# Performance work log

Hardware: AMD Instinct MI355X
Metric: run time of the kernel (lower is better)

Reference implementation:

```python
import jax, jax.numpy as jnp
import numpy as np

EMBED_DIM = 256
NUM_HEADS = 4
LN_EPS = 1e-5


def setup_inputs() -> dict:
    b, n, e = 2, 4096, EMBED_DIM
    key = jax.random.key(0)
    ks = jax.random.split(key, 12)
    x = jax.random.normal(ks[0], (b, n, e), dtype=jnp.float32)
    # rotary cache: cos/sin of random angles, shape [2, b, n, e, 1]
    ang = jax.random.uniform(ks[1], (b, n, e, 1), dtype=jnp.float32) * (2 * np.pi)
    encoding = jnp.stack([jnp.cos(ang), jnp.sin(ang)], axis=0)
    s_e = 1.0 / np.sqrt(e)
    s_2e = 1.0 / np.sqrt(2 * e)
    Wqkv_w = jax.random.normal(ks[2], (3 * e, e), dtype=jnp.float32) * s_e
    Wqkv_b = jax.random.normal(ks[3], (3 * e,), dtype=jnp.float32) * s_e
    out_w = jax.random.normal(ks[4], (e, e), dtype=jnp.float32) * s_e
    out_b = jax.random.normal(ks[5], (e,), dtype=jnp.float32) * s_e
    ffn1_w = jax.random.normal(ks[6], (2 * e, 2 * e), dtype=jnp.float32) * s_2e
    ffn1_b = jax.random.normal(ks[7], (2 * e,), dtype=jnp.float32) * s_2e
    ln_g = jnp.ones((2 * e,), dtype=jnp.float32)
    ln_b = jnp.zeros((2 * e,), dtype=jnp.float32)
    ffn2_w = jax.random.normal(ks[8], (e, 2 * e), dtype=jnp.float32) * s_2e
    ffn2_b = jax.random.normal(ks[9], (e,), dtype=jnp.float32) * s_2e
    return {"x": x, "encoding": encoding, "Wqkv_w": Wqkv_w, "Wqkv_b": Wqkv_b,
            "out_w": out_w, "out_b": out_b, "ffn1_w": ffn1_w, "ffn1_b": ffn1_b,
            "ln_g": ln_g, "ln_b": ln_b, "ffn2_w": ffn2_w, "ffn2_b": ffn2_b}


def _forward(x, encoding, Wqkv_w, Wqkv_b, out_w, out_b, ffn1_w, ffn1_b, ln_g, ln_b, ffn2_w, ffn2_b):
    b, n, e = x.shape
    h = NUM_HEADS
    hd = e // h
    qkv = x @ Wqkv_w.T + Wqkv_b                      # [b,n,3e]
    qkv = qkv.reshape(b, n, e, 3)
    qk, v = qkv[..., :2], qkv[..., 2]                # [b,n,e,2], [b,n,e]
    # rotate_half: interpret e as (h, hd//2, 2) pairs, rotate within pairs
    r = qk.reshape(b, n, h, hd // 2, 2, 2)
    r = jnp.stack([-r[..., 1, :], r[..., 0, :]], axis=4).reshape(b, n, e, 2)
    qk = qk * encoding[0] + r * encoding[1]          # cached rotary emb
    q = qk[..., 0].reshape(b, n, h, hd)
    k = qk[..., 1].reshape(b, n, h, hd)
    vh = v.reshape(b, n, h, hd)
    scale = 1.0 / np.sqrt(hd).astype(np.float32)
    scores = jnp.einsum('bqhd,bkhd->bhqk', q, k) * scale
    attn = jax.nn.softmax(scores, axis=-1)
    ctx = jnp.einsum('bhqk,bkhd->bqhd', attn, vh).reshape(b, n, e)
    message = ctx @ out_w.T + out_b
    y = jnp.concatenate([x, message], axis=2)        # [b,n,2e]
    y = y @ ffn1_w.T + ffn1_b
    mu = jnp.mean(y, axis=-1, keepdims=True)
    var = jnp.mean(jnp.square(y - mu), axis=-1, keepdims=True)
    y = (y - mu) * jax.lax.rsqrt(var + LN_EPS) * ln_g + ln_b
    y = jax.nn.gelu(y, approximate=False)            # torch nn.GELU default = exact
    y = y @ ffn2_w.T + ffn2_b
    return x + y


def reference(x, encoding, Wqkv_w, Wqkv_b, out_w, out_b, ffn1_w, ffn1_b, ln_g, ln_b, ffn2_w, ffn2_b):
    return _forward(x, encoding, Wqkv_w, Wqkv_b, out_w, out_b, ffn1_w, ffn1_b, ln_g, ln_b, ffn2_w, ffn2_b)
```

## Files before the change

### kernel.cpp

```cpp
#include <hip/hip_runtime.h>
#include <hip/hip_bf16.h>

using u16 = unsigned short;
using u16x8 = __attribute__((ext_vector_type(8))) unsigned short;
using s16x4 = __attribute__((ext_vector_type(4))) short;
using s16x8 = __attribute__((ext_vector_type(8))) short;
using f32x4 = __attribute__((ext_vector_type(4))) float;

__device__ __forceinline__ f32x4 mfma16(s16x8 a, s16x8 b, f32x4 c) {
    return __builtin_amdgcn_mfma_f32_16x16x32_bf16(a, b, c, 0, 0, 0);
}

__device__ __forceinline__ u16 f2bf(float f) {
    union { float f; unsigned u; } v; v.f = f;
    unsigned r = v.u + 0x7FFFu + ((v.u >> 16) & 1u);
    return (u16)(r >> 16);
}

__device__ __forceinline__ unsigned cvt_pk_bf16(float lo, float hi) {
    unsigned r;
    asm("v_cvt_pk_bf16_f32 %0, %1, %2" : "=v"(r) : "v"(lo), "v"(hi));
    return r;
}

__device__ __forceinline__ float fast_exp2(float x) {
    float r;
    asm("v_exp_f32 %0, %1" : "=v"(r) : "v"(x));
    return r;
}

__device__ __forceinline__ unsigned pk2(u16 a, u16 b) {
    return (unsigned)a | ((unsigned)b << 16);
}

__device__ __forceinline__ float bf2f(u16 u) {
    union { unsigned u; float f; } v; v.u = ((unsigned)u) << 16;
    return v.f;
}

__device__ __forceinline__ void gload_lds16(const u16* g, u16* l) {
    __builtin_amdgcn_global_load_lds(
        (const __attribute__((address_space(1))) void*)g,
        (__attribute__((address_space(3))) void*)l, 16, 0, 0);
}

__global__ __launch_bounds__(256) void conv_kernel(
    const float* __restrict__ s0, const float* __restrict__ s1,
    const float* __restrict__ s2, const float* __restrict__ s3,
    const float* __restrict__ s4,
    u16* __restrict__ d0, u16* __restrict__ d1, u16* __restrict__ d2,
    u16* __restrict__ d3, u16* __restrict__ d4)
{
    int i = blockIdx.x * 256 + threadIdx.x;
    const float* s; u16* d; int off;
    if (i < 524288)      { s = s0; d = d0; off = i; }
    else if (i < 573440) { s = s1; d = d1; off = i - 524288; }
    else if (i < 589824) { s = s2; d = d2; off = i - 573440; }
    else if (i < 655360) { s = s3; d = d3; off = i - 589824; }
    else                 { s = s4; d = d4; off = i - 655360; }
    float4 f = ((const float4*)s)[off];
    ushort4 u;
    u.x = f2bf(f.x); u.y = f2bf(f.y); u.z = f2bf(f.z); u.w = f2bf(f.w);
    ((ushort4*)d)[off] = u;
}

__global__ __launch_bounds__(256) void prep_kernel(
    const float* __restrict__ wout, const float* __restrict__ w1,
    const float* __restrict__ outb, const float* __restrict__ b1,
    u16* __restrict__ woutT, float* __restrict__ b1p)
{
    int bid = blockIdx.x, tid = threadIdx.x;
    if (bid < 16) {
        __shared__ u16 ts[64][72];
        int tr = (bid >> 2) * 64, tc = (bid & 3) * 64;
        #pragma unroll
        for (int i = 0; i < 2; ++i) {
            int c = tid + 256 * i;
            int r = c >> 3, cg = c & 7;
            float4 fa = *(const float4*)(wout + (size_t)(tr + r) * 256 + tc + cg * 8);
            float4 fb = *(const float4*)(wout + (size_t)(tr + r) * 256 + tc + cg * 8 + 4);
            ts[r][cg * 8 + 0] = f2bf(fa.x); ts[r][cg * 8 + 1] = f2bf(fa.y);
            ts[r][cg * 8 + 2] = f2bf(fa.z); ts[r][cg * 8 + 3] = f2bf(fa.w);
            ts[r][cg * 8 + 4] = f2bf(fb.x); ts[r][cg * 8 + 5] = f2bf(fb.y);
            ts[r][cg * 8 + 6] = f2bf(fb.z); ts[r][cg * 8 + 7] = f2bf(fb.w);
        }
        __syncthreads();
        #pragma unroll
        for (int i = 0; i < 2; ++i) {
            int c = tid + 256 * i;
            int d = c >> 3, ng = c & 7;
            uint4 o4 = make_uint4(
                pk2(ts[ng*8+0][d], ts[ng*8+1][d]), pk2(ts[ng*8+2][d], ts[ng*8+3][d]),
                pk2(ts[ng*8+4][d], ts[ng*8+5][d]), pk2(ts[ng*8+6][d], ts[ng*8+7][d]));
            *(uint4*)(woutT + (size_t)(tc + d) * 256 + tr + ng * 8) = o4;
        }
    } else {
        #pragma unroll
        for (int h = 0; h < 2; ++h) {
            int n = tid + 256 * h;
            float acc = b1[n];
            const float* wr = w1 + (size_t)n * 512 + 256;
            for (int k = 0; k < 256; ++k) acc += wr[k] * outb[k];
            b1p[n] = acc;
        }
    }
}

template<int OUTMODE, bool SPLIT, bool SPLITW, bool RESID, bool BIAS, int BM>
__global__ __launch_bounds__(256) void gemm_kernel(
    const u16* __restrict__ A0, const u16* __restrict__ A1,
    const u16* __restrict__ W0, const u16* __restrict__ W1,
    const float* __restrict__ bias, const float* __restrict__ resid,
    float* __restrict__ outf, u16* __restrict__ outb,
    int M, int N, int K, int lda0, int lda1, int ldw0, int ldw1, int ldo)
{
    constexpr int MS = BM / 32;
    __shared__ u16 A_lds[3][BM][64];
    __shared__ u16 B_lds[3][64][64];
    const int tid = threadIdx.x;
    const int l = tid & 63, w = tid >> 6;
    const int lr = l & 15, lg = l >> 4;
    const int r7 = lr & 7;
    const int m0 = blockIdx.x * BM, n0 = blockIdx.y * 64;
    const int wm = (w >> 1) * (BM / 2), wn = (w & 1) * 32;

    const int lrow = l >> 3;
    const int swz = (l & 7) ^ lrow;
    const int arow = (BM / 4) * w + lrow;
    const int brow = 16 * w + lrow;

    #define STAGE_G(s, b)                                                     \
        do {                                                                  \
            int k0_ = 64 * (s);                                               \
            const u16* As_; int lda_; int ka_ = k0_;                          \
            if (SPLIT && k0_ >= 256) { As_ = A1; lda_ = lda1; ka_ = k0_ - 256; }\
            else { As_ = A0; lda_ = lda0; }                                   \
            const u16* Ws_; int ldw_; int kw_ = k0_;                          \
            if (SPLITW && k0_ >= 256) { Ws_ = W1; ldw_ = ldw1; kw_ = k0_ - 256; }\
            else { Ws_ = W0; ldw_ = ldw0; }                                   \
            _Pragma("unroll")                                                 \
            for (int i = 0; i < BM / 32; ++i)                                 \
                gload_lds16(As_ + (size_t)(m0 + arow + 8 * i) * lda_ + ka_ + swz * 8,\
                            &A_lds[b][(BM / 4) * w + 8 * i][0]);              \
            _Pragma("unroll")                                                 \
            for (int i = 0; i < 2; ++i)                                       \
                gload_lds16(Ws_ + (size_t)(n0 + brow + 8 * i) * ldw_ + kw_ + swz * 8,\
                            &B_lds[b][16 * w + 8 * i][0]);                    \
        } while (0)

    f32x4 acc[MS][2];
    #pragma unroll
    for (int i = 0; i < MS; ++i)
        #pragma unroll
        for (int j = 0; j < 2; ++j)
            acc[i][j] = (f32x4){0.f, 0.f, 0.f, 0.f};

    const int NS = K >> 6;
    int cur = 0, nxt = 1;
    STAGE_G(0, 0);

    for (int s = 0; s < NS; ++s) {
        if (s + 1 < NS) {
            STAGE_G(s + 1, nxt);
            if constexpr (BM == 128)
                asm volatile("s_waitcnt vmcnt(6)" ::: "memory");
            else
                asm volatile("s_waitcnt vmcnt(4)" ::: "memory");
        } else {
            asm volatile("s_waitcnt vmcnt(0)" ::: "memory");
        }
        __builtin_amdgcn_sched_barrier(0);
        __builtin_amdgcn_s_barrier();
        __builtin_amdgcn_sched_barrier(0);

        #pragma unroll
        for (int ks = 0; ks < 2; ++ks) {
            s16x8 af[MS], bfr[2];
            #pragma unroll
            for (int ms = 0; ms < MS; ++ms)
                af[ms] = *(const s16x8*)&A_lds[cur][wm + ms * 16 + lr]
                                              [((ks * 4 + lg) ^ r7) * 8];
            #pragma unroll
            for (int ns = 0; ns < 2; ++ns)
                bfr[ns] = *(const s16x8*)&B_lds[cur][wn + ns * 16 + lr]
                                               [((ks * 4 + lg) ^ r7) * 8];
            #pragma unroll
            for (int ms = 0; ms < MS; ++ms)
                #pragma unroll
                for (int ns = 0; ns < 2; ++ns)
                    acc[ms][ns] = mfma16(af[ms], bfr[ns], acc[ms][ns]);
        }
        cur = nxt;
        nxt = (nxt == 2) ? 0 : nxt + 1;
    }
    #undef STAGE_G

    #pragma unroll
    for (int ms = 0; ms < MS; ++ms) {
        #pragma unroll
        for (int ns = 0; ns < 2; ++ns) {
            int cg = n0 + wn + ns * 16 + lr;
            float bv = BIAS ? bias[cg] : 0.f;
            #pragma unroll
            for (int r = 0; r < 4; ++r) {
                int rg = m0 + wm + ms * 16 + lg * 4 + r;
                float val = acc[ms][ns][r] + bv;
                if (RESID) val += resid[(size_t)rg * N + cg];
                if (OUTMODE == 0) outf[(size_t)rg * ldo + cg] = val;
                else              outb[(size_t)rg * ldo + cg] = f2bf(val);
            }
        }
    }
}

__global__ __launch_bounds__(256) void rope_tv_kernel(
    const u16* __restrict__ qkv, const float* __restrict__ enc,
    u16* __restrict__ Qo, u16* __restrict__ Ko, u16* __restrict__ Vt)
{
    __shared__ u16 vt_lds[64][72];
    const int tid = threadIdx.x;
    const int bh = blockIdx.y, n0 = blockIdx.x * 64;
    const int b = bh >> 2, h = bh & 3;
    const float qs = 0.18033688011112042f;

    #pragma unroll
    for (int it = 0; it < 8; ++it) {
        int task = it * 256 + tid;
        int r = task >> 5, t = task & 31;
        size_t grow = (size_t)(b * 4096 + n0 + r);
        const u16* base = qkv + grow * 768 + 3 * (h * 64) + 6 * t;
        ushort2 a01 = *(const ushort2*)(base);
        ushort2 a23 = *(const ushort2*)(base + 2);
        ushort2 a45 = *(const ushort2*)(base + 4);
        float q0 = bf2f(a01.x), k0 = bf2f(a01.y);
        float q1 = bf2f(a23.y), k1 = bf2f(a45.x);
        const float* cb = enc + grow * 256 + h * 64 + 2 * t;
        float2 cosv = *(const float2*)cb;
        float2 sinv = *(const float2*)(cb + 2097152);
        float qr0 = (q0 * cosv.x - q1 * sinv.x) * qs;
        float qr1 = (q1 * cosv.y + q0 * sinv.y) * qs;
        float kr0 = k0 * cosv.x - k1 * sinv.x;
        float kr1 = k1 * cosv.y + k0 * sinv.y;
        size_t o = ((size_t)bh * 4096 + n0 + r) * 64 + 2 * t;
        *(unsigned*)(Qo + o) = cvt_pk_bf16(qr0, qr1);
        *(unsigned*)(Ko + o) = cvt_pk_bf16(kr0, kr1);
        vt_lds[r][2 * t]     = a23.x;
        vt_lds[r][2 * t + 1] = a45.y;
    }
    __syncthreads();
    #pragma unroll
    for (int i = 0; i < 2; ++i) {
        int c = tid + 256 * i;
        int d = c >> 3, ng = c & 7;
        int kb = ng >> 2, lg4 = ng & 3;
        int base = 32 * kb + 4 * lg4;
        unsigned w0 = pk2(vt_lds[base +  0][d], vt_lds[base +  1][d]);
        unsigned w1 = pk2(vt_lds[base +  2][d], vt_lds[base +  3][d]);
        unsigned w2 = pk2(vt_lds[base + 16][d], vt_lds[base + 17][d]);
        unsigned w3 = pk2(vt_lds[base + 18][d], vt_lds[base + 19][d]);
        uint4 o4 = make_uint4(w0, w1, w2, w3);
        *(uint4*)(Vt + ((size_t)bh * 64 + d) * 4096 + n0 + ng * 8) = o4;
    }
}

__global__ __launch_bounds__(256) void attn_kernel(
    const u16* __restrict__ Qp, const u16* __restrict__ Kp,
    const u16* __restrict__ Vtp, u16* __restrict__ Opart,
    float* __restrict__ Ssum)
{
    __shared__ u16 K_lds[2][64][64];
    __shared__ u16 V_lds[2][64][64];
    const int tid = threadIdx.x;
    const int l = tid & 63, w = tid >> 6;
    const int lr = l & 15, lg = l >> 4;
    const int r7 = lr & 7;
    const int bh = blockIdx.y, z = blockIdx.z;
    const int n0 = blockIdx.x * 128 + w * 32;

    const u16* Qb = Qp + ((size_t)bh * 4096 + n0) * 64;
    s16x8 qf[2][2];
    #pragma unroll
    for (int qt = 0; qt < 2; ++qt)
        #pragma unroll
        for (int dh = 0; dh < 2; ++dh)
            qf[qt][dh] = *(const s16x8*)(Qb + (qt * 16 + lr) * 64 + dh * 32 + lg * 8);

    const u16* Kb = Kp + (size_t)bh * 4096 * 64 + (size_t)z * 1024 * 64;
    const u16* Vb = Vtp + (size_t)bh * 64 * 4096 + z * 1024;

    const int xs0 = (lg ^ r7) * 8;
    const int xs1 = ((4 + lg) ^ r7) * 8;

    const int swz = (l & 7) ^ ((l >> 3) & 7);
    const int row0 = 16 * w + (l >> 3);
    const size_t koff0 = (size_t)row0 * 64 + swz * 8;
    const size_t koff1 = (size_t)(row0 + 8) * 64 + swz * 8;
    const size_t voff0 = (size_t)row0 * 4096 + swz * 8;
    const size_t voff1 = (size_t)(row0 + 8) * 4096 + swz * 8;

    #define STAGE(kt, b)                                                      \
        do {                                                                  \
            const u16* ks_ = Kb + (size_t)(kt) * 4096;                        \
            const u16* vs_ = Vb + (size_t)(kt) * 64;                          \
            gload_lds16(ks_ + koff0, &K_lds[b][16 * w][0]);                   \
            gload_lds16(ks_ + koff1, &K_lds[b][16 * w + 8][0]);               \
            gload_lds16(vs_ + voff0, &V_lds[b][16 * w][0]);                   \
            gload_lds16(vs_ + voff1, &V_lds[b][16 * w + 8][0]);               \
        } while (0)

    f32x4 O[2][4];
    #pragma unroll
    for (int qt = 0; qt < 2; ++qt)
        #pragma unroll
        for (int dv = 0; dv < 4; ++dv)
            O[qt][dv] = (f32x4){0.f, 0.f, 0.f, 0.f};
    f32x4 ssum[2];
    ssum[0] = (f32x4){0.f, 0.f, 0.f, 0.f};
    ssum[1] = (f32x4){0.f, 0.f, 0.f, 0.f};
    s16x8 ones;
    #pragma unroll
    for (int j = 0; j < 8; ++j) ones[j] = (short)0x3F80;

    STAGE(0, 0);
    __syncthreads();

    #define PHASE(kt, CB, DO_STAGE)                                           \
        do {                                                                  \
            if (DO_STAGE) STAGE((kt) + 1, (CB) ^ 1);                          \
            f32x4 S[2][4];                                                    \
            __builtin_amdgcn_s_setprio(1);                                    \
            _Pragma("unroll")                                                 \
            for (int v4 = 0; v4 < 4; ++v4) {                                  \
                const int krow = v4 * 16 + lr;                                \
                s16x8 kf0 = *(const s16x8*)&K_lds[CB][krow][xs0];             \
                s16x8 kf1 = *(const s16x8*)&K_lds[CB][krow][xs1];             \
                _Pragma("unroll")                                             \
                for (int qt = 0; qt < 2; ++qt) {                              \
                    f32x4 zz = (f32x4){-24.f, -24.f, -24.f, -24.f};           \
                    zz = mfma16(kf0, qf[qt][0], zz);                          \
                    zz = mfma16(kf1, qf[qt][1], zz);                          \
                    S[qt][v4] = zz;                                           \
                }                                                             \
            }                                                                 \
            __builtin_amdgcn_s_setprio(0);                                    \
            s16x8 pa[2][2];                                                   \
            _Pragma("unroll")                                                 \
            for (int qt = 0; qt < 2; ++qt) {                                  \
                float p[4][4];                                                \
                _Pragma("unroll")                                             \
                for (int v4 = 0; v4 < 4; ++v4)                                \
                    _Pragma("unroll")                                         \
                    for (int r = 0; r < 4; ++r)                               \
                        p[v4][r] = fast_exp2(S[qt][v4][r]);                   \
                _Pragma("unroll")                                             \
                for (int kb = 0; kb < 2; ++kb) {                              \
                    union { unsigned u[4]; s16x8 v; } pu;                     \
                    pu.u[0] = cvt_pk_bf16(p[2*kb][0],   p[2*kb][1]);          \
                    pu.u[1] = cvt_pk_bf16(p[2*kb][2],   p[2*kb][3]);          \
                    pu.u[2] = cvt_pk_bf16(p[2*kb+1][0], p[2*kb+1][1]);        \
                    pu.u[3] = cvt_pk_bf16(p[2*kb+1][2], p[2*kb+1][3]);        \
                    pa[qt][kb] = pu.v;                                        \
                }                                                             \
            }                                                                 \
            __builtin_amdgcn_s_setprio(1);                                    \
            _Pragma("unroll")                                                 \
            for (int dv = 0; dv < 4; ++dv) {                                  \
                const int vrow = 16 * dv + lr;                                \
                s16x8 vf0 = *(const s16x8*)&V_lds[CB][vrow][xs0];             \
                s16x8 vf1 = *(const s16x8*)&V_lds[CB][vrow][xs1];             \
                _Pragma("unroll")                                             \
                for (int qt = 0; qt < 2; ++qt) {                              \
                    O[qt][dv] = mfma16(pa[qt][0], vf0, O[qt][dv]);            \
                    O[qt][dv] = mfma16(pa[qt][1], vf1, O[qt][dv]);            \
                }                                                             \
            }                                                                 \
            _Pragma("unroll")                                                 \
            for (int qt = 0; qt < 2; ++qt) {                                  \
                ssum[qt] = mfma16(pa[qt][0], ones, ssum[qt]);                 \
                ssum[qt] = mfma16(pa[qt][1], ones, ssum[qt]);                 \
            }                                                                 \
            __builtin_amdgcn_s_setprio(0);                                    \
            __syncthreads();                                                  \
        } while (0)

    #pragma unroll 1
    for (int kt = 0; kt < 16; kt += 2) {
        PHASE(kt, 0, true);
        PHASE(kt + 1, 1, kt < 14);
    }
    #undef PHASE
    #undef STAGE

    u16* Ob = Opart + ((size_t)(z * 8 + bh) * 4096 + n0) * 64;
    #pragma unroll
    for (int qt = 0; qt < 2; ++qt)
        #pragma unroll
        for (int dv = 0; dv < 4; ++dv)
            #pragma unroll
            for (int r = 0; r < 4; ++r)
                Ob[(size_t)(qt * 16 + 4 * lg + r) * 64 + 16 * dv + lr] =
                    f2bf(O[qt][dv][r]);
    if (lr == 0) {
        #pragma unroll
        for (int qt = 0; qt < 2; ++qt) {
            float4 sv = make_float4(ssum[qt][0], ssum[qt][1],
                                    ssum[qt][2], ssum[qt][3]);
            *(float4*)&Ssum[(size_t)(z * 8 + bh) * 4096 + n0 + qt * 16 + 4 * lg] = sv;
        }
    }
}

__global__ __launch_bounds__(256) void combine_kernel(
    const u16* __restrict__ Opart, const float* __restrict__ Ssum,
    u16* __restrict__ ctx)
{
    int idx = blockIdx.x * 256 + threadIdx.x;
    int rr = idx >> 3;
    int dc = (idx & 7) * 8;
    float s = Ssum[rr] + Ssum[32768 + rr] + Ssum[65536 + rr] + Ssum[98304 + rr];
    float inv = 1.f / s;
    float acc[8];
    #pragma unroll
    for (int j = 0; j < 8; ++j) acc[j] = 0.f;
    #pragma unroll
    for (int z = 0; z < 4; ++z) {
        u16x8 ov = *(const u16x8*)(Opart + ((size_t)z * 32768 + rr) * 64 + dc);
        #pragma unroll
        for (int j = 0; j < 8; ++j) acc[j] += bf2f(ov[j]);
    }
    #pragma unroll
    for (int j = 0; j < 8; ++j) acc[j] *= inv;
    int bh = rr >> 12, n = rr & 4095;
    int b = bh >> 2, h = bh & 3;
    uint4 o4 = make_uint4(cvt_pk_bf16(acc[0], acc[1]), cvt_pk_bf16(acc[2], acc[3]),
                          cvt_pk_bf16(acc[4], acc[5]), cvt_pk_bf16(acc[6], acc[7]));
    *(uint4*)(ctx + ((size_t)(b * 4096 + n)) * 256 + h * 64 + dc) = o4;
}

__global__ __launch_bounds__(256) void ln_gelu_kernel(
    const u16* __restrict__ y, const float* __restrict__ g,
    const float* __restrict__ bta, u16* __restrict__ o)
{
    int row = blockIdx.x * 4 + (threadIdx.x >> 6);
    int l = threadIdx.x & 63;
    const u16* yr = y + (size_t)row * 512 + l * 8;
    u16x8 uv = *(const u16x8*)yr;
    float v[8];
    #pragma unroll
    for (int j = 0; j < 8; ++j) v[j] = bf2f(uv[j]);
    float s = 0.f;
    #pragma unroll
    for (int j = 0; j < 8; ++j) s += v[j];
    #pragma unroll
    for (int off = 32; off; off >>= 1) s += __shfl_xor(s, off, 64);
    float mu = s * (1.f / 512.f);
    float q = 0.f;
    #pragma unroll
    for (int j = 0; j < 8; ++j) { float t = v[j] - mu; q += t * t; }
    #pragma unroll
    for (int off = 32; off; off >>= 1) q += __shfl_xor(q, off, 64);
    float rs = rsqrtf(q * (1.f / 512.f) + 1e-5f);
    u16 u[8];
    #pragma unroll
    for (int j = 0; j < 8; ++j) {
        float t = (v[j] - mu) * rs * g[l * 8 + j] + bta[l * 8 + j];
        t = t * 0.5f * (1.f + erff(t * 0.70710678118654752f));
        u[j] = f2bf(t);
    }
    uint4 o4 = make_uint4(pk2(u[0], u[1]), pk2(u[2], u[3]),
                          pk2(u[4], u[5]), pk2(u[6], u[7]));
    *(uint4*)(o + (size_t)row * 512 + l * 8) = o4;
}

extern "C" void kernel_launch(void* const* d_in, const int* in_sizes, int n_in,
                              void* d_out, int out_size, void* d_ws, size_t ws_size,
                              hipStream_t stream) {
    (void)in_sizes; (void)n_in; (void)out_size; (void)ws_size;
    const float* x    = (const float*)d_in[0];
    const float* enc  = (const float*)d_in[1];
    const float* wqkv = (const float*)d_in[2];
    const float* bqkv = (const float*)d_in[3];
    const float* wout = (const float*)d_in[4];
    const float* bout = (const float*)d_in[5];
    const float* w1   = (const float*)d_in[6];
    const float* b1   = (const float*)d_in[7];
    const float* lng  = (const float*)d_in[8];
    const float* lnb  = (const float*)d_in[9];
    const float* w2   = (const float*)d_in[10];
    const float* b2   = (const float*)d_in[11];
    float* out = (float*)d_out;
    char* ws = (char*)d_ws;

    u16*   xb    = (u16*)(ws + 0);
    u16*   wqkvb = (u16*)(ws + 4194304);
    u16*   woutb = (u16*)(ws + 4587520);
    u16*   w1b   = (u16*)(ws + 4718592);
    u16*   w2b   = (u16*)(ws + 5242880);
    u16*   qkvb  = (u16*)(ws + 5505024);
    u16*   OpartB= (u16*)(ws + 5505024);
    u16*   y1bf  = (u16*)(ws + 5505024);
    float* Ssum  = (float*)(ws + 22282240);
    u16*   woutT = (u16*)(ws + 22806528);
    u16*   wprime= (u16*)(ws + 22937600);
    float* b1p   = (float*)(ws + 23199744);
    u16*   q     = (u16*)(ws + 30670848);
    u16*   k     = (u16*)(ws + 34865152);
    u16*   vt    = (u16*)(ws + 43253760);
    u16*   ybf   = q;
    u16*   ctx   = (u16*)(ws + 47448064);

    conv_kernel<<<2688, 256, 0, stream>>>(x, wqkv, wout, w1, w2,
                                          xb, wqkvb, woutb, w1b, w2b);
    prep_kernel<<<17, 256, 0, stream>>>(wout, w1, bout, b1, woutT, b1p);
    gemm_kernel<1, false, false, false, false, 64><<<dim3(8, 4), 256, 0, stream>>>(
        w1b + 256, nullptr, woutT, nullptr, nullptr, nullptr, nullptr, wprime,
        512, 256, 256, 512, 0, 256, 0, 256);
    gemm_kernel<1, false, false, false, true, 128><<<dim3(64, 12), 256, 0, stream>>>(
        xb, nullptr, wqkvb, nullptr, bqkv, nullptr, nullptr, qkvb,
        8192, 768, 256, 256, 0, 256, 0, 768);
    rope_tv_kernel<<<dim3(64, 8), 256, 0, stream>>>(qkvb, enc, q, k, vt);
    attn_kernel<<<dim3(32, 8, 4), 256, 0, stream>>>(q, k, vt, OpartB, Ssum);
    combine_kernel<<<1024, 256, 0, stream>>>(OpartB, Ssum, ctx);
    gemm_kernel<1, true, true, false, true, 128><<<dim3(64, 8), 256, 0, stream>>>(
        xb, ctx, w1b, wprime, b1p, nullptr, nullptr, y1bf,
        8192, 512, 512, 256, 256, 512, 256, 512);
    ln_gelu_kernel<<<2048, 256, 0, stream>>>(y1bf, lng, lnb, ybf);
    gemm_kernel<0, false, false, true, true, 64><<<dim3(128, 4), 256, 0, stream>>>(
        ybf, nullptr, w2b, nullptr, b2, x, out, nullptr,
        8192, 256, 512, 512, 0, 512, 0, 256);
}
```

Before: 132.9 us.

## Replace folded out-projection weights with an explicit out-projection GEMM

Removes the precomputed folding of the output projection into the first FFN weights (the prep kernel, the W1·Wout GEMM and the folded bias). It instead runs a separate out-projection GEMM from ctx to a bf16 message buffer, then feeds x and the message into the FFN1 GEMM with the original weights and bias. This drops two small weight-prep launches and the split-weight path in the GEMM. In exchange it adds an 8192x256x256 GEMM plus a round trip of the message tensor through memory.

```diff
diff --git a/kernel.cpp b/kernel.cpp
--- a/kernel.cpp
+++ b/kernel.cpp
@@ -64,55 +64,13 @@
     ((ushort4*)d)[off] = u;
 }
 
-__global__ __launch_bounds__(256) void prep_kernel(
-    const float* __restrict__ wout, const float* __restrict__ w1,
-    const float* __restrict__ outb, const float* __restrict__ b1,
-    u16* __restrict__ woutT, float* __restrict__ b1p)
-{
-    int bid = blockIdx.x, tid = threadIdx.x;
-    if (bid < 16) {
-        __shared__ u16 ts[64][72];
-        int tr = (bid >> 2) * 64, tc = (bid & 3) * 64;
-        #pragma unroll
-        for (int i = 0; i < 2; ++i) {
-            int c = tid + 256 * i;
-            int r = c >> 3, cg = c & 7;
-            float4 fa = *(const float4*)(wout + (size_t)(tr + r) * 256 + tc + cg * 8);
-            float4 fb = *(const float4*)(wout + (size_t)(tr + r) * 256 + tc + cg * 8 + 4);
-            ts[r][cg * 8 + 0] = f2bf(fa.x); ts[r][cg * 8 + 1] = f2bf(fa.y);
-            ts[r][cg * 8 + 2] = f2bf(fa.z); ts[r][cg * 8 + 3] = f2bf(fa.w);
-            ts[r][cg * 8 + 4] = f2bf(fb.x); ts[r][cg * 8 + 5] = f2bf(fb.y);
-            ts[r][cg * 8 + 6] = f2bf(fb.z); ts[r][cg * 8 + 7] = f2bf(fb.w);
-        }
-        __syncthreads();
-        #pragma unroll
-        for (int i = 0; i < 2; ++i) {
-            int c = tid + 256 * i;
-            int d = c >> 3, ng = c & 7;
-            uint4 o4 = make_uint4(
-                pk2(ts[ng*8+0][d], ts[ng*8+1][d]), pk2(ts[ng*8+2][d], ts[ng*8+3][d]),
-                pk2(ts[ng*8+4][d], ts[ng*8+5][d]), pk2(ts[ng*8+6][d], ts[ng*8+7][d]));
-            *(uint4*)(woutT + (size_t)(tc + d) * 256 + tr + ng * 8) = o4;
-        }
-    } else {
-        #pragma unroll
-        for (int h = 0; h < 2; ++h) {
-            int n = tid + 256 * h;
-            float acc = b1[n];
-            const float* wr = w1 + (size_t)n * 512 + 256;
-            for (int k = 0; k < 256; ++k) acc += wr[k] * outb[k];
-            b1p[n] = acc;
-        }
-    }
-}
-
-template<int OUTMODE, bool SPLIT, bool SPLITW, bool RESID, bool BIAS, int BM>
+template<int OUTMODE, bool SPLIT, bool RESID, bool BIAS, int BM>
 __global__ __launch_bounds__(256) void gemm_kernel(
     const u16* __restrict__ A0, const u16* __restrict__ A1,
-    const u16* __restrict__ W0, const u16* __restrict__ W1,
-    const float* __restrict__ bias, const float* __restrict__ resid,
-    float* __restrict__ outf, u16* __restrict__ outb,
-    int M, int N, int K, int lda0, int lda1, int ldw0, int ldw1, int ldo)
+    const u16* __restrict__ W0, const float* __restrict__ bias,
+    const float* __restrict__ resid, float* __restrict__ outf,
+    u16* __restrict__ outb,
+    int M, int N, int K, int lda0, int lda1, int ldw0, int ldo)
 {
     constexpr int MS = BM / 32;
     __shared__ u16 A_lds[3][BM][64];
@@ -135,16 +93,13 @@
             const u16* As_; int lda_; int ka_ = k0_;                          \
             if (SPLIT && k0_ >= 256) { As_ = A1; lda_ = lda1; ka_ = k0_ - 256; }\
             else { As_ = A0; lda_ = lda0; }                                   \
-            const u16* Ws_; int ldw_; int kw_ = k0_;                          \
-            if (SPLITW && k0_ >= 256) { Ws_ = W1; ldw_ = ldw1; kw_ = k0_ - 256; }\
-            else { Ws_ = W0; ldw_ = ldw0; }                                   \
             _Pragma("unroll")                                                 \
             for (int i = 0; i < BM / 32; ++i)                                 \
                 gload_lds16(As_ + (size_t)(m0 + arow + 8 * i) * lda_ + ka_ + swz * 8,\
                             &A_lds[b][(BM / 4) * w + 8 * i][0]);              \
             _Pragma("unroll")                                                 \
             for (int i = 0; i < 2; ++i)                                       \
-                gload_lds16(Ws_ + (size_t)(n0 + brow + 8 * i) * ldw_ + kw_ + swz * 8,\
+                gload_lds16(W0 + (size_t)(n0 + brow + 8 * i) * ldw0 + k0_ + swz * 8,\
                             &B_lds[b][16 * w + 8 * i][0]);                    \
         } while (0)
 
@@ -500,32 +455,29 @@
     u16*   OpartB= (u16*)(ws + 5505024);
     u16*   y1bf  = (u16*)(ws + 5505024);
     float* Ssum  = (float*)(ws + 22282240);
-    u16*   woutT = (u16*)(ws + 22806528);
-    u16*   wprime= (u16*)(ws + 22937600);
-    float* b1p   = (float*)(ws + 23199744);
     u16*   q     = (u16*)(ws + 30670848);
     u16*   k     = (u16*)(ws + 34865152);
     u16*   vt    = (u16*)(ws + 43253760);
     u16*   ybf   = q;
     u16*   ctx   = (u16*)(ws + 47448064);
+    u16*   msg   = (u16*)(ws + 51642368);
 
     conv_kernel<<<2688, 256, 0, stream>>>(x, wqkv, wout, w1, w2,
                                           xb, wqkvb, woutb, w1b, w2b);
-    prep_kernel<<<17, 256, 0, stream>>>(wout, w1, bout, b1, woutT, b1p);
-    gemm_kernel<1, false, false, false, false, 64><<<dim3(8, 4), 256, 0, stream>>>(
-        w1b + 256, nullptr, woutT, nullptr, nullptr, nullptr, nullptr, wprime,
-        512, 256, 256, 512, 0, 256, 0, 256);
-    gemm_kernel<1, false, false, false, true, 128><<<dim3(64, 12), 256, 0, stream>>>(
-        xb, nullptr, wqkvb, nullptr, bqkv, nullptr, nullptr, qkvb,
-        8192, 768, 256, 256, 0, 256, 0, 768);
+    gemm_kernel<1, false, false, true, 128><<<dim3(64, 12), 256, 0, stream>>>(
+        xb, nullptr, wqkvb, bqkv, nullptr, nullptr, qkvb,
+        8192, 768, 256, 256, 0, 256, 768);
     rope_tv_kernel<<<dim3(64, 8), 256, 0, stream>>>(qkvb, enc, q, k, vt);
     attn_kernel<<<dim3(32, 8, 4), 256, 0, stream>>>(q, k, vt, OpartB, Ssum);
     combine_kernel<<<1024, 256, 0, stream>>>(OpartB, Ssum, ctx);
-    gemm_kernel<1, true, true, false, true, 128><<<dim3(64, 8), 256, 0, stream>>>(
-        xb, ctx, w1b, wprime, b1p, nullptr, nullptr, y1bf,
-        8192, 512, 512, 256, 256, 512, 256, 512);
+    gemm_kernel<1, false, false, true, 64><<<dim3(128, 4), 256, 0, stream>>>(
+        ctx, nullptr, woutb, bout, nullptr, nullptr, msg,
+        8192, 256, 256, 256, 0, 256, 256);
+    gemm_kernel<1, true, false, true, 128><<<dim3(64, 8), 256, 0, stream>>>(
+        xb, msg, w1b, b1, nullptr, nullptr, y1bf,
+        8192, 512, 512, 256, 256, 512, 512);
     ln_gelu_kernel<<<2048, 256, 0, stream>>>(y1bf, lng, lnb, ybf);
-    gemm_kernel<0, false, false, true, true, 64><<<dim3(128, 4), 256, 0, stream>>>(
-        ybf, nullptr, w2b, nullptr, b2, x, out, nullptr,
-        8192, 256, 512, 512, 0, 512, 0, 256);
-}
+    gemm_kernel<0, false, true, true, 64><<<dim3(128, 4), 256, 0, stream>>>(
+        ybf, nullptr, w2b, b2, x, out, nullptr,
+        8192, 256, 512, 512, 0, 512, 256);
+}
```

Measured after the change: 116.5 us. 12.3% less time.
